# Optimization experiments

Hardware: AMD Instinct MI355X
Metric: run time of the kernel (lower is better)

## Reference

```python
import jax, jax.numpy as jnp
import numpy as np

N, E, D, R, G, C = 100000, 600000, 128, 4, 256, 16
EPS = 1e-5

def _rgcn(x, src, dst, edge_type, w_rel, w_root, b):
    # out_i = x_i @ W_root + b + sum_r mean_{j in N_r(i)} x_j @ W_r  (PyG RGCNConv, aggr='mean')
    x_src = x[src]                                   # [E, D] gather
    out = x @ w_root + b                             # [N, D]
    for r in range(R):
        m = (edge_type == r).astype(x.dtype)         # [E]
        msg = (x_src @ w_rel[r]) * m[:, None]        # [E, D]
        agg = jax.ops.segment_sum(msg, dst, num_segments=N)
        cnt = jax.ops.segment_sum(m, dst, num_segments=N)
        out = out + agg / jnp.maximum(cnt, 1.0)[:, None]
    return out

def _bn_eval(x, gamma, beta, mean, var):
    return (x - mean) * jax.lax.rsqrt(var + EPS) * gamma + beta

def setup_inputs() -> dict:
    key = jax.random.key(0)
    ks = jax.random.split(key, 12)
    x = jax.random.normal(ks[0], (N, D), dtype=jnp.float32)
    edge_index = jax.random.randint(ks[1], (2, E), 0, N)
    edge_type = jax.random.randint(ks[2], (E,), 0, R)
    batch = jnp.sort(jax.random.randint(ks[3], (N,), 0, G))
    s = 1.0 / np.sqrt(D)
    conv_rel_w = jax.random.normal(ks[4], (3, R, D, D), dtype=jnp.float32) * s
    conv_root_w = jax.random.normal(ks[5], (3, D, D), dtype=jnp.float32) * s
    conv_bias = jnp.zeros((3, D), dtype=jnp.float32)
    bn_gamma = jnp.ones((2, D), dtype=jnp.float32)
    bn_beta = jnp.zeros((2, D), dtype=jnp.float32)
    bn_mean = jax.random.normal(ks[6], (2, D), dtype=jnp.float32) * 0.1
    bn_var = jax.random.uniform(ks[7], (2, D), minval=0.5, maxval=1.5, dtype=jnp.float32)
    cls_w1 = jax.random.normal(ks[8], (D, D // 2), dtype=jnp.float32) * s
    cls_b1 = jnp.zeros((D // 2,), dtype=jnp.float32)
    cls_w2 = jax.random.normal(ks[9], (D // 2, C), dtype=jnp.float32) / np.sqrt(D // 2)
    cls_b2 = jnp.zeros((C,), dtype=jnp.float32)
    return {"x": x, "edge_index": edge_index, "edge_type": edge_type, "batch": batch,
            "conv_rel_w": conv_rel_w, "conv_root_w": conv_root_w, "conv_bias": conv_bias,
            "bn_gamma": bn_gamma, "bn_beta": bn_beta, "bn_mean": bn_mean, "bn_var": bn_var,
            "cls_w1": cls_w1, "cls_b1": cls_b1, "cls_w2": cls_w2, "cls_b2": cls_b2}

def reference(x, edge_index, edge_type, batch, conv_rel_w, conv_root_w, conv_bias,
              bn_gamma, bn_beta, bn_mean, bn_var, cls_w1, cls_b1, cls_w2, cls_b2):
    src, dst = edge_index[0], edge_index[1]
    prev = None
    h = x
    for i in range(3):
        h_new = _rgcn(h, src, dst, edge_type, conv_rel_w[i], conv_root_w[i], conv_bias[i])
        if prev is not None:
            h_new = h_new + prev  # residual (shapes always match: D==D)
        if i != 2:
            h_new = _bn_eval(h_new, bn_gamma[i], bn_beta[i], bn_mean[i], bn_var[i])
            h_new = jax.nn.elu(h_new)  # alpha=1; dropout inactive in eval
        prev = h_new
        h = h_new
    # global mean pool over graphs
    sums = jax.ops.segment_sum(h, batch, num_segments=G)          # [G, D]
    cnts = jax.ops.segment_sum(jnp.ones((N,), h.dtype), batch, num_segments=G)
    pooled = sums / jnp.maximum(cnts, 1.0)[:, None]
    z = jax.nn.elu(pooled @ cls_w1 + cls_b1)
    logits = z @ cls_w2 + cls_b2
    return jax.nn.log_softmax(logits, axis=-1)
```

## Files before the change

kernel.cpp:

```cpp
#include <hip/hip_runtime.h>
#include <hip/hip_bf16.h>

#define NN 100000
#define EE 600000
#define DD 128
#define GG 256
#define CCL 16

typedef __attribute__((ext_vector_type(8))) short short8;
typedef __attribute__((ext_vector_type(4))) float f32x4;
typedef const __attribute__((address_space(1))) void* gas_t;
typedef __attribute__((address_space(3))) void* las_t;

__device__ __forceinline__ void async_ld16(const void* g, void* l) {
    __builtin_amdgcn_global_load_lds((gas_t)g, (las_t)l, 16, 0, 0);
}
__device__ __forceinline__ unsigned short f2bf(float x) {
    unsigned u = __float_as_uint(x);
    unsigned r = (u + 0x7FFFu + ((u >> 16) & 1u)) >> 16;
    return (unsigned short)r;
}
__device__ __forceinline__ float bf2f(unsigned short b) {
    return __uint_as_float(((unsigned)b) << 16);
}
__device__ __forceinline__ void unpack8(uint4 v, float* f) {
    f[0] = __uint_as_float(v.x << 16); f[1] = __uint_as_float(v.x & 0xFFFF0000u);
    f[2] = __uint_as_float(v.y << 16); f[3] = __uint_as_float(v.y & 0xFFFF0000u);
    f[4] = __uint_as_float(v.z << 16); f[5] = __uint_as_float(v.z & 0xFFFF0000u);
    f[6] = __uint_as_float(v.w << 16); f[7] = __uint_as_float(v.w & 0xFFFF0000u);
}

__global__ __launch_bounds__(256) void sniff_kernel(const void* __restrict__ xraw, int* __restrict__ flag) {
    int t = threadIdx.x;
    const unsigned short* u = (const unsigned short*)xraw;
    int good = 0;
    #pragma unroll
    for (int i = 0; i < 4; i++) {
        unsigned short b = u[t * 4 + i];
        int e = (b >> 7) & 0xFF;
        if (e >= 107 && e <= 130) good++;
    }
    __shared__ int sg[256];
    sg[t] = good;
    __syncthreads();
    for (int s = 128; s > 0; s >>= 1) { if (t < s) sg[t] += sg[t + s]; __syncthreads(); }
    if (t == 0) flag[0] = (sg[0] >= 900) ? 1 : 0;
}

__device__ __forceinline__ float loadf(const void* p, size_t i, int isbf) {
    if (isbf) return bf2f(((const unsigned short*)p)[i]);
    return ((const float*)p)[i];
}

__global__ __launch_bounds__(256) void convx_kernel(const void* __restrict__ xraw, const int* __restrict__ flag,
                                                    __hip_bfloat16* __restrict__ xc) {
    int isbf = flag[0];
    size_t i0 = ((size_t)blockIdx.x * 256 + threadIdx.x) * 8;
    if (i0 >= (size_t)NN * DD) return;
    if (isbf) {
        *(uint4*)(xc + i0) = *(const uint4*)((const __hip_bfloat16*)xraw + i0);
    } else {
        const float* xf = (const float*)xraw;
        unsigned short o[8];
        #pragma unroll
        for (int j = 0; j < 8; j++) o[j] = f2bf(xf[i0 + j]);
        *(uint4*)(xc + i0) = *(uint4*)o;
    }
}

__global__ __launch_bounds__(256) void convw_kernel(const void* __restrict__ rel_raw, const void* __restrict__ root_raw,
                                                    const int* __restrict__ flag, __hip_bfloat16* __restrict__ wt) {
    int isbf = flag[0];
    int mat = blockIdx.x;
    int layer = mat / 5, g = mat % 5;
    size_t srcoff = (g == 0) ? (size_t)layer * 16384 : (size_t)(layer * 4 + (g - 1)) * 16384;
    const void* sraw = (g == 0) ? root_raw : rel_raw;
    __hip_bfloat16* dstp = wt + (size_t)mat * 16384;
    for (int idx = threadIdx.x; idx < 16384; idx += 256) {
        int k = idx >> 7, n = idx & 127;
        float v = loadf(sraw, srcoff + (size_t)k * 128 + n, isbf);
        dstp[n * 128 + k] = __float2bfloat16(v);
    }
}

__global__ __launch_bounds__(256) void convp_kernel(const void* bias, const void* bng, const void* bnb,
                                                    const void* bnm, const void* bnv, const void* w1,
                                                    const void* b1, const void* w2, const void* b2,
                                                    const int* __restrict__ flag, float* __restrict__ pf) {
    int isbf = flag[0];
    int b = blockIdx.x, t = threadIdx.x;
    if (b < 9) {
        const void* srcs[9] = {bias, bng, bnb, bnm, bnv, w1, b1, w2, b2};
        const int cnts[9] = {384, 256, 256, 256, 256, 8192, 64, 1024, 16};
        const int offs[9] = {0, 384, 640, 896, 1152, 1408, 9600, 9664, 10688};
        const void* s = srcs[b];
        int c = cnts[b], o = offs[b];
        for (int i = t; i < c; i += 256) pf[o + i] = loadf(s, i, isbf);
    } else {
        int bl = b - 9;
        if (t < 128) {
            float iva = rsqrtf(loadf(bnv, bl * 128 + t, isbf) + 1e-5f);
            float gm = loadf(bng, bl * 128 + t, isbf) * iva;
            float ga = loadf(bnb, bl * 128 + t, isbf) - loadf(bnm, bl * 128 + t, isbf) * gm;
            pf[11008 + bl * 256 + t] = gm;
            pf[11008 + bl * 256 + 128 + t] = ga;
        }
    }
}

__global__ __launch_bounds__(256) void count4_kernel(const int* __restrict__ dst, const int* __restrict__ et,
                                                     int* __restrict__ cnt4) {
    int e = blockIdx.x * 256 + threadIdx.x;
    if (e < EE) atomicAdd(&cnt4[dst[e] * 4 + et[e]], 1);
}

__global__ __launch_bounds__(256) void allocn_kernel(const int* __restrict__ cnt4, int* __restrict__ counter,
                                                     int* __restrict__ startn, int* __restrict__ wptrn) {
    int n = blockIdx.x * 256 + threadIdx.x;
    int lane = threadIdx.x & 63;
    int c = 0;
    if (n < NN) {
        int4 cv = *(const int4*)(cnt4 + n * 4);
        c = cv.x + cv.y + cv.z + cv.w;
    }
    int v = c;
    #pragma unroll
    for (int d = 1; d < 64; d <<= 1) {
        int o = __shfl_up(v, d);
        if (lane >= d) v += o;
    }
    int base = 0;
    if (lane == 63) base = atomicAdd(counter, v);
    base = __shfl(base, 63);
    if (n < NN) {
        int s = base + v - c;
        startn[n] = s;
        wptrn[n] = s;
    }
}

__global__ __launch_bounds__(256) void filln_kernel(const int* __restrict__ src, const int* __restrict__ dst,
                                                    const int* __restrict__ et, const int* __restrict__ cnt4,
                                                    int* __restrict__ wptrn, int2* __restrict__ ewe) {
    int e = blockIdx.x * 256 + threadIdx.x;
    if (e < EE) {
        int d = dst[e], r = et[e];
        float w = 1.f / (float)cnt4[d * 4 + r];
        int pos = atomicAdd(&wptrn[d], 1);
        ewe[pos] = make_int2(src[e] * 512 + r * 128, __float_as_int(w));
    }
}

__global__ __launch_bounds__(256) void gemmy_kernel(const __hip_bfloat16* __restrict__ h_in,
                                                    const __hip_bfloat16* __restrict__ wt5,
                                                    __hip_bfloat16* __restrict__ Yroot,
                                                    __hip_bfloat16* __restrict__ Yrel) {
    __shared__ __align__(16) short lds[16384];
    int t = threadIdx.x;
    int wave = t >> 6, lane = t & 63, quad = lane >> 4, r16 = lane & 15;
    int m0 = blockIdx.x * 128;
    int g = blockIdx.y;

    const __hip_bfloat16* wg = wt5 + (size_t)g * 16384;
    #pragma unroll
    for (int j = 0; j < 8; j++) {
        int slot = j * 256 + t;
        int brow = slot >> 4, sp = slot & 15;
        async_ld16(wg + brow * 128 + (sp ^ (brow & 15)) * 8, &lds[slot * 8]);
    }
    int r0 = m0 + wave * 32 + r16;      if (r0 > NN - 1) r0 = NN - 1;
    int r1 = m0 + wave * 32 + 16 + r16; if (r1 > NN - 1) r1 = NN - 1;
    const __hip_bfloat16* ap0 = h_in + (size_t)r0 * 128;
    const __hip_bfloat16* ap1 = h_in + (size_t)r1 * 128;
    short8 a0[4], a1[4];
    #pragma unroll
    for (int kc = 0; kc < 4; kc++) {
        a0[kc] = *(const short8*)(ap0 + kc * 32 + quad * 8);
        a1[kc] = *(const short8*)(ap1 + kc * 32 + quad * 8);
    }
    __syncthreads();

    f32x4 acc[2][8];
    #pragma unroll
    for (int i = 0; i < 2; i++)
        #pragma unroll
        for (int j = 0; j < 8; j++) acc[i][j] = (f32x4){0.f, 0.f, 0.f, 0.f};
    #pragma unroll
    for (int kc = 0; kc < 4; kc++) {
        int s = kc * 4 + quad;
        #pragma unroll
        for (int nt = 0; nt < 8; nt++) {
            int rb = nt * 16 + r16;
            short8 b = *(const short8*)&lds[(rb * 16 + (s ^ (rb & 15))) * 8];
            acc[0][nt] = __builtin_amdgcn_mfma_f32_16x16x32_bf16(a0[kc], b, acc[0][nt], 0, 0, 0);
            acc[1][nt] = __builtin_amdgcn_mfma_f32_16x16x32_bf16(a1[kc], b, acc[1][nt], 0, 0, 0);
        }
    }
    __syncthreads();

    #pragma unroll
    for (int nt = 0; nt < 8; nt++) {
        int col = nt * 16 + r16;
        #pragma unroll
        for (int mt = 0; mt < 2; mt++) {
            #pragma unroll
            for (int reg = 0; reg < 4; reg++) {
                int crow = wave * 32 + mt * 16 + quad * 4 + reg;
                int sslot = (col >> 3) ^ (crow & 15);
                lds[crow * 128 + sslot * 8 + (col & 7)] = (short)f2bf(acc[mt][nt][reg]);
            }
        }
    }
    __syncthreads();

    #pragma unroll
    for (int it = 0; it < 8; it++) {
        int u4 = it * 256 + t;
        int crow = u4 >> 4, seg = u4 & 15;
        int node = m0 + crow;
        if (node < NN) {
            int sslot = seg ^ (crow & 15);
            short8 cv = *(const short8*)&lds[crow * 128 + sslot * 8];
            __hip_bfloat16* dp = (g == 0) ? (Yroot + (size_t)node * 128 + seg * 8)
                                          : (Yrel + (size_t)node * 512 + (g - 1) * 128 + seg * 8);
            *(uint4*)dp = *(uint4*)&cv;
        }
    }
}

__global__ __launch_bounds__(256) void sagg_kernel(const __hip_bfloat16* __restrict__ Yrel,
                                                   const __hip_bfloat16* __restrict__ Yroot,
                                                   const int2* __restrict__ ewe,
                                                   const int* __restrict__ startn,
                                                   const int* __restrict__ wptrn,
                                                   const float* __restrict__ bias,
                                                   const float* __restrict__ gmp,
                                                   const float* __restrict__ gap,
                                                   const __hip_bfloat16* __restrict__ hres,
                                                   __hip_bfloat16* __restrict__ hout,
                                                   int do_bn) {
    int node = blockIdx.x * 16 + (threadIdx.x >> 4);
    int c16 = threadIdx.x & 15;
    int s = startn[node];
    int c = wptrn[node] - s;
    int col0 = c16 * 8;
    float a[8];
    unpack8(*(const uint4*)(Yroot + (size_t)node * 128 + col0), a);
    int i = 0;
    for (; i + 8 <= c; i += 8) {
        int2 ee[8];
        uint4 vv[8];
        #pragma unroll
        for (int q = 0; q < 8; q++) ee[q] = ewe[s + i + q];
        #pragma unroll
        for (int q = 0; q < 8; q++) vv[q] = *(const uint4*)(Yrel + ee[q].x + col0);
        #pragma unroll
        for (int q = 0; q < 8; q++) {
            float w = __int_as_float(ee[q].y);
            float f[8];
            unpack8(vv[q], f);
            #pragma unroll
            for (int j = 0; j < 8; j++) a[j] += w * f[j];
        }
    }
    for (; i + 4 <= c; i += 4) {
        int2 ee[4];
        uint4 vv[4];
        #pragma unroll
        for (int q = 0; q < 4; q++) ee[q] = ewe[s + i + q];
        #pragma unroll
        for (int q = 0; q < 4; q++) vv[q] = *(const uint4*)(Yrel + ee[q].x + col0);
        #pragma unroll
        for (int q = 0; q < 4; q++) {
            float w = __int_as_float(ee[q].y);
            float f[8];
            unpack8(vv[q], f);
            #pragma unroll
            for (int j = 0; j < 8; j++) a[j] += w * f[j];
        }
    }
    for (; i < c; i++) {
        int2 e0 = ewe[s + i];
        uint4 v0 = *(const uint4*)(Yrel + e0.x + col0);
        float w0 = __int_as_float(e0.y);
        float f0[8];
        unpack8(v0, f0);
        #pragma unroll
        for (int j = 0; j < 8; j++) a[j] += w0 * f0[j];
    }
    if (hres) {
        float rf[8];
        unpack8(*(const uint4*)(hres + (size_t)node * 128 + col0), rf);
        #pragma unroll
        for (int j = 0; j < 8; j++) a[j] = a[j] + bias[col0 + j] + rf[j];
    } else {
        #pragma unroll
        for (int j = 0; j < 8; j++) a[j] = a[j] + bias[col0 + j];
    }
    if (do_bn) {
        #pragma unroll
        for (int j = 0; j < 8; j++) {
            float z = a[j] * gmp[col0 + j] + gap[col0 + j];
            a[j] = z > 0.f ? z : expm1f(z);
        }
    }
    unsigned short u[8];
    #pragma unroll
    for (int j = 0; j < 8; j++) u[j] = f2bf(a[j]);
    *(uint4*)(hout + (size_t)node * 128 + col0) = *(uint4*)u;
}

__global__ __launch_bounds__(256) void pool_kernel(const __hip_bfloat16* __restrict__ h3,
                                                   const int* __restrict__ batch,
                                                   float* __restrict__ pooled) {
    int g = blockIdx.x, t = threadIdx.x;
    int rowpar = t >> 4, colg = t & 15;
    int lo = 0, hi = NN;
    while (lo < hi) { int mid = (lo + hi) >> 1; if (batch[mid] < g) lo = mid + 1; else hi = mid; }
    int s0 = lo;
    hi = NN;
    while (lo < hi) { int mid = (lo + hi) >> 1; if (batch[mid] < g + 1) lo = mid + 1; else hi = mid; }
    int s1 = lo;
    float a[8];
    #pragma unroll
    for (int j = 0; j < 8; j++) a[j] = 0.f;
    for (int n = s0 + rowpar; n < s1; n += 16) {
        float f[8];
        unpack8(*(const uint4*)(h3 + (size_t)n * 128 + colg * 8), f);
        #pragma unroll
        for (int j = 0; j < 8; j++) a[j] += f[j];
    }
    __shared__ float sd[16][128];
    #pragma unroll
    for (int j = 0; j < 8; j++) sd[rowpar][colg * 8 + j] = a[j];
    __syncthreads();
    if (t < 128) {
        float sum = 0.f;
        #pragma unroll
        for (int i = 0; i < 16; i++) sum += sd[i][t];
        int cgn = s1 - s0;
        pooled[g * 128 + t] = sum / (float)(cgn > 0 ? cgn : 1);
    }
}

__global__ __launch_bounds__(64) void cls_kernel(const float* __restrict__ pooled,
                                                 const float* __restrict__ pf,
                                                 const int* __restrict__ flag,
                                                 void* __restrict__ out) {
    int g = blockIdx.x, j = threadIdx.x;
    const float* w1 = pf + 1408;
    const float* b1 = pf + 9600;
    const float* w2 = pf + 9664;
    const float* b2 = pf + 10688;
    __shared__ float z[64];
    __shared__ float lg[16];
    const float* p = pooled + g * 128;
    float acc = b1[j];
    for (int d = 0; d < 128; d++) acc += p[d] * w1[d * 64 + j];
    acc = acc > 0.f ? acc : expm1f(acc);
    z[j] = acc;
    __syncthreads();
    if (j < CCL) {
        float l = b2[j];
        for (int k = 0; k < 64; k++) l += z[k] * w2[k * 16 + j];
        lg[j] = l;
    }
    __syncthreads();
    if (j < CCL) {
        float m = lg[0];
        for (int k = 1; k < CCL; k++) m = fmaxf(m, lg[k]);
        float s = 0.f;
        for (int k = 0; k < CCL; k++) s += expf(lg[k] - m);
        float val = lg[j] - m - logf(s);
        if (flag[0]) ((__hip_bfloat16*)out)[g * CCL + j] = __float2bfloat16(val);
        else         ((float*)out)[g * CCL + j] = val;
    }
}

extern "C" void kernel_launch(void* const* d_in, const int* in_sizes, int n_in,
                              void* d_out, int out_size, void* d_ws, size_t ws_size,
                              hipStream_t stream) {
    const void* x_raw    = d_in[0];
    const int* ei        = (const int*)d_in[1];
    const int* et        = (const int*)d_in[2];
    const int* batch     = (const int*)d_in[3];
    const void* rel_raw  = d_in[4];
    const void* root_raw = d_in[5];
    const int* srcp = ei;
    const int* dstp = ei + EE;

    char* ws = (char*)d_ws;
    size_t off = 0;
    auto take = [&](size_t bytes) { size_t r = off; off += (bytes + 1023) & ~(size_t)1023; return r; };
    __hip_bfloat16* Yrel  = (__hip_bfloat16*)(ws + take((size_t)NN * 512 * 2));
    __hip_bfloat16* Yroot = (__hip_bfloat16*)(ws + take((size_t)NN * 128 * 2));
    __hip_bfloat16* xc    = (__hip_bfloat16*)(ws + take((size_t)NN * 128 * 2));
    __hip_bfloat16* hA    = (__hip_bfloat16*)(ws + take((size_t)NN * 128 * 2));
    __hip_bfloat16* hB    = (__hip_bfloat16*)(ws + take((size_t)NN * 128 * 2));
    __hip_bfloat16* hC    = (__hip_bfloat16*)(ws + take((size_t)NN * 128 * 2));
    __hip_bfloat16* wt    = (__hip_bfloat16*)(ws + take((size_t)15 * 16384 * 2));
    float* pf             = (float*)(ws + take((size_t)11520 * 4));
    float* pooled         = (float*)(ws + take((size_t)GG * 128 * 4));
    int* cnt4             = (int*)(ws + take((size_t)NN * 16 + 8));
    int* counter          = cnt4 + NN * 4;
    int* flag             = cnt4 + NN * 4 + 1;
    int* startn           = (int*)(ws + take((size_t)NN * 4));
    int* wptrn            = (int*)(ws + take((size_t)NN * 4));
    int2* ewe             = (int2*)(ws + take((size_t)EE * 8));

    hipMemsetAsync(cnt4, 0, (size_t)NN * 16 + 4, stream);
    sniff_kernel<<<1, 256, 0, stream>>>(x_raw, flag);
    convx_kernel<<<(NN * DD / 8 + 255) / 256, 256, 0, stream>>>(x_raw, flag, xc);
    convw_kernel<<<15, 256, 0, stream>>>(rel_raw, root_raw, flag, wt);
    convp_kernel<<<11, 256, 0, stream>>>(d_in[6], d_in[7], d_in[8], d_in[9], d_in[10],
                                         d_in[11], d_in[12], d_in[13], d_in[14], flag, pf);
    count4_kernel<<<(EE + 255) / 256, 256, 0, stream>>>(dstp, et, cnt4);
    allocn_kernel<<<(NN + 255) / 256, 256, 0, stream>>>(cnt4, counter, startn, wptrn);
    filln_kernel<<<(EE + 255) / 256, 256, 0, stream>>>(srcp, dstp, et, cnt4, wptrn, ewe);

    const __hip_bfloat16* hin = xc;
    __hip_bfloat16* houts[3] = {hA, hB, hC};
    dim3 ggrid((NN + 127) / 128, 5);
    for (int l = 0; l < 3; l++) {
        int bl = l < 2 ? l : 1;
        gemmy_kernel<<<ggrid, 256, 0, stream>>>(hin, wt + (size_t)l * 5 * 16384, Yroot, Yrel);
        sagg_kernel<<<NN / 16, 256, 0, stream>>>(
            Yrel, Yroot, ewe, startn, wptrn, pf + l * 128,
            pf + 11008 + bl * 256, pf + 11008 + bl * 256 + 128,
            (l > 0) ? hin : (const __hip_bfloat16*)nullptr, houts[l], (l < 2) ? 1 : 0);
        hin = houts[l];
    }
    pool_kernel<<<GG, 256, 0, stream>>>(houts[2], batch, pooled);
    cls_kernel<<<GG, 64, 0, stream>>>(pooled, pf, flag, (void*)d_out);
}
```

Before: 576.8 us.

## Aggregate neighbors before transform, fuse K=640 GEMM with bias/BN/ELU epilogue

Reorders each RGCN layer so per-relation mean aggregation of raw 128-wide features happens first, with edges bucketed by (dst, relation). A single GEMM then multiplies the concatenated [h | A_0..A_3] by the stacked weights, and bias, residual, BN and ELU are applied in its epilogue. This replaces the gather of 512-wide transformed rows and the separate Yroot/Yrel writes with 128-wide gathers and one fused output pass. The edge record shrinks to a source index, and the normalisation weight is taken from the per-bucket count. The cost is an extra Abuf write and read per layer and serialised K chunks inside each GEMM block.

New measurement: 572.7 us. Within noise of the previous version (-0.7%).

```diff
diff --git a/kernel.cpp b/kernel.cpp
--- a/kernel.cpp
+++ b/kernel.cpp
@@ -115,12 +115,13 @@
 }
 
 __global__ __launch_bounds__(256) void allocn_kernel(const int* __restrict__ cnt4, int* __restrict__ counter,
-                                                     int* __restrict__ startn, int* __restrict__ wptrn) {
+                                                     int* __restrict__ startn, int* __restrict__ wptr4) {
     int n = blockIdx.x * 256 + threadIdx.x;
     int lane = threadIdx.x & 63;
+    int4 cv = make_int4(0, 0, 0, 0);
     int c = 0;
     if (n < NN) {
-        int4 cv = *(const int4*)(cnt4 + n * 4);
+        cv = *(const int4*)(cnt4 + n * 4);
         c = cv.x + cv.y + cv.z + cv.w;
     }
     int v = c;
@@ -135,179 +136,182 @@
     if (n < NN) {
         int s = base + v - c;
         startn[n] = s;
-        wptrn[n] = s;
-    }
-}
-
-__global__ __launch_bounds__(256) void filln_kernel(const int* __restrict__ src, const int* __restrict__ dst,
-                                                    const int* __restrict__ et, const int* __restrict__ cnt4,
-                                                    int* __restrict__ wptrn, int2* __restrict__ ewe) {
+        wptr4[n * 4 + 0] = s;
+        wptr4[n * 4 + 1] = s + cv.x;
+        wptr4[n * 4 + 2] = s + cv.x + cv.y;
+        wptr4[n * 4 + 3] = s + cv.x + cv.y + cv.z;
+    }
+}
+
+__global__ __launch_bounds__(256) void fill4_kernel(const int* __restrict__ src, const int* __restrict__ dst,
+                                                    const int* __restrict__ et, int* __restrict__ wptr4,
+                                                    int* __restrict__ esrc) {
     int e = blockIdx.x * 256 + threadIdx.x;
     if (e < EE) {
-        int d = dst[e], r = et[e];
-        float w = 1.f / (float)cnt4[d * 4 + r];
-        int pos = atomicAdd(&wptrn[d], 1);
-        ewe[pos] = make_int2(src[e] * 512 + r * 128, __float_as_int(w));
-    }
-}
-
-__global__ __launch_bounds__(256) void gemmy_kernel(const __hip_bfloat16* __restrict__ h_in,
+        int pos = atomicAdd(&wptr4[dst[e] * 4 + et[e]], 1);
+        esrc[pos] = src[e];
+    }
+}
+
+__global__ __launch_bounds__(256) void agg_kernel(const __hip_bfloat16* __restrict__ h,
+                                                  const int* __restrict__ esrc,
+                                                  const int* __restrict__ startn,
+                                                  const int* __restrict__ cnt4,
+                                                  __hip_bfloat16* __restrict__ Abuf) {
+    int node = blockIdx.x * 16 + (threadIdx.x >> 4);
+    int c16 = threadIdx.x & 15;
+    int col0 = c16 * 8;
+    int4 cv = *(const int4*)(cnt4 + node * 4);
+    int s = startn[node];
+    int cr[4] = {cv.x, cv.y, cv.z, cv.w};
+    #pragma unroll
+    for (int r = 0; r < 4; r++) {
+        int c = cr[r];
+        float a[8];
+        #pragma unroll
+        for (int j = 0; j < 8; j++) a[j] = 0.f;
+        int i = 0;
+        for (; i + 4 <= c; i += 4) {
+            int s4[4];
+            uint4 vv[4];
+            #pragma unroll
+            for (int q = 0; q < 4; q++) s4[q] = esrc[s + i + q];
+            #pragma unroll
+            for (int q = 0; q < 4; q++) vv[q] = *(const uint4*)(h + (size_t)s4[q] * 128 + col0);
+            #pragma unroll
+            for (int q = 0; q < 4; q++) {
+                float f[8];
+                unpack8(vv[q], f);
+                #pragma unroll
+                for (int j = 0; j < 8; j++) a[j] += f[j];
+            }
+        }
+        for (; i < c; i++) {
+            int sq = esrc[s + i];
+            uint4 v0 = *(const uint4*)(h + (size_t)sq * 128 + col0);
+            float f[8];
+            unpack8(v0, f);
+            #pragma unroll
+            for (int j = 0; j < 8; j++) a[j] += f[j];
+        }
+        float w = (c > 0) ? (1.f / (float)c) : 0.f;
+        unsigned short u[8];
+        #pragma unroll
+        for (int j = 0; j < 8; j++) u[j] = f2bf(a[j] * w);
+        *(uint4*)(Abuf + (size_t)node * 512 + r * 128 + col0) = *(uint4*)u;
+        s += c;
+    }
+}
+
+__global__ __launch_bounds__(256) void rgemm_kernel(const __hip_bfloat16* __restrict__ h_in,
+                                                    const __hip_bfloat16* __restrict__ Abuf,
                                                     const __hip_bfloat16* __restrict__ wt5,
-                                                    __hip_bfloat16* __restrict__ Yroot,
-                                                    __hip_bfloat16* __restrict__ Yrel) {
+                                                    const float* __restrict__ bias,
+                                                    const float* __restrict__ gmp,
+                                                    const float* __restrict__ gap,
+                                                    const __hip_bfloat16* __restrict__ hres,
+                                                    __hip_bfloat16* __restrict__ hout,
+                                                    int do_bn) {
     __shared__ __align__(16) short lds[16384];
     int t = threadIdx.x;
     int wave = t >> 6, lane = t & 63, quad = lane >> 4, r16 = lane & 15;
     int m0 = blockIdx.x * 128;
-    int g = blockIdx.y;
-
-    const __hip_bfloat16* wg = wt5 + (size_t)g * 16384;
-    #pragma unroll
-    for (int j = 0; j < 8; j++) {
-        int slot = j * 256 + t;
-        int brow = slot >> 4, sp = slot & 15;
-        async_ld16(wg + brow * 128 + (sp ^ (brow & 15)) * 8, &lds[slot * 8]);
-    }
+
     int r0 = m0 + wave * 32 + r16;      if (r0 > NN - 1) r0 = NN - 1;
     int r1 = m0 + wave * 32 + 16 + r16; if (r1 > NN - 1) r1 = NN - 1;
-    const __hip_bfloat16* ap0 = h_in + (size_t)r0 * 128;
-    const __hip_bfloat16* ap1 = h_in + (size_t)r1 * 128;
-    short8 a0[4], a1[4];
-    #pragma unroll
-    for (int kc = 0; kc < 4; kc++) {
-        a0[kc] = *(const short8*)(ap0 + kc * 32 + quad * 8);
-        a1[kc] = *(const short8*)(ap1 + kc * 32 + quad * 8);
-    }
-    __syncthreads();
 
     f32x4 acc[2][8];
     #pragma unroll
     for (int i = 0; i < 2; i++)
         #pragma unroll
         for (int j = 0; j < 8; j++) acc[i][j] = (f32x4){0.f, 0.f, 0.f, 0.f};
-    #pragma unroll
-    for (int kc = 0; kc < 4; kc++) {
-        int s = kc * 4 + quad;
-        #pragma unroll
-        for (int nt = 0; nt < 8; nt++) {
-            int rb = nt * 16 + r16;
-            short8 b = *(const short8*)&lds[(rb * 16 + (s ^ (rb & 15))) * 8];
-            acc[0][nt] = __builtin_amdgcn_mfma_f32_16x16x32_bf16(a0[kc], b, acc[0][nt], 0, 0, 0);
-            acc[1][nt] = __builtin_amdgcn_mfma_f32_16x16x32_bf16(a1[kc], b, acc[1][nt], 0, 0, 0);
-        }
-    }
-    __syncthreads();
-
-    #pragma unroll
-    for (int nt = 0; nt < 8; nt++) {
-        int col = nt * 16 + r16;
-        #pragma unroll
-        for (int mt = 0; mt < 2; mt++) {
-            #pragma unroll
-            for (int reg = 0; reg < 4; reg++) {
-                int crow = wave * 32 + mt * 16 + quad * 4 + reg;
-                int sslot = (col >> 3) ^ (crow & 15);
-                lds[crow * 128 + sslot * 8 + (col & 7)] = (short)f2bf(acc[mt][nt][reg]);
+
+    #pragma unroll
+    for (int ch = 0; ch < 5; ch++) {
+        if (ch) __syncthreads();
+        const __hip_bfloat16* wg = wt5 + (size_t)ch * 16384;
+        #pragma unroll
+        for (int j = 0; j < 8; j++) {
+            int slot = j * 256 + t;
+            int brow = slot >> 4, sp = slot & 15;
+            async_ld16(wg + brow * 128 + (sp ^ (brow & 15)) * 8, &lds[slot * 8]);
+        }
+        const __hip_bfloat16* ap0;
+        const __hip_bfloat16* ap1;
+        if (ch == 0) {
+            ap0 = h_in + (size_t)r0 * 128;
+            ap1 = h_in + (size_t)r1 * 128;
+        } else {
+            ap0 = Abuf + (size_t)r0 * 512 + (ch - 1) * 128;
+            ap1 = Abuf + (size_t)r1 * 512 + (ch - 1) * 128;
+        }
+        short8 a0[4], a1[4];
+        #pragma unroll
+        for (int kc = 0; kc < 4; kc++) {
+            a0[kc] = *(const short8*)(ap0 + kc * 32 + quad * 8);
+            a1[kc] = *(const short8*)(ap1 + kc * 32 + quad * 8);
+        }
+        __syncthreads();
+        #pragma unroll
+        for (int kc = 0; kc < 4; kc++) {
+            int s = kc * 4 + quad;
+            #pragma unroll
+            for (int nt = 0; nt < 8; nt++) {
+                int rb = nt * 16 + r16;
+                short8 b = *(const short8*)&lds[(rb * 16 + (s ^ (rb & 15))) * 8];
+                acc[0][nt] = __builtin_amdgcn_mfma_f32_16x16x32_bf16(a0[kc], b, acc[0][nt], 0, 0, 0);
+                acc[1][nt] = __builtin_amdgcn_mfma_f32_16x16x32_bf16(a1[kc], b, acc[1][nt], 0, 0, 0);
             }
         }
     }
-    __syncthreads();
-
-    #pragma unroll
-    for (int it = 0; it < 8; it++) {
-        int u4 = it * 256 + t;
-        int crow = u4 >> 4, seg = u4 & 15;
-        int node = m0 + crow;
-        if (node < NN) {
-            int sslot = seg ^ (crow & 15);
-            short8 cv = *(const short8*)&lds[crow * 128 + sslot * 8];
-            __hip_bfloat16* dp = (g == 0) ? (Yroot + (size_t)node * 128 + seg * 8)
-                                          : (Yrel + (size_t)node * 512 + (g - 1) * 128 + seg * 8);
-            *(uint4*)dp = *(uint4*)&cv;
-        }
-    }
-}
-
-__global__ __launch_bounds__(256) void sagg_kernel(const __hip_bfloat16* __restrict__ Yrel,
-                                                   const __hip_bfloat16* __restrict__ Yroot,
-                                                   const int2* __restrict__ ewe,
-                                                   const int* __restrict__ startn,
-                                                   const int* __restrict__ wptrn,
-                                                   const float* __restrict__ bias,
-                                                   const float* __restrict__ gmp,
-                                                   const float* __restrict__ gap,
-                                                   const __hip_bfloat16* __restrict__ hres,
-                                                   __hip_bfloat16* __restrict__ hout,
-                                                   int do_bn) {
-    int node = blockIdx.x * 16 + (threadIdx.x >> 4);
-    int c16 = threadIdx.x & 15;
-    int s = startn[node];
-    int c = wptrn[node] - s;
-    int col0 = c16 * 8;
-    float a[8];
-    unpack8(*(const uint4*)(Yroot + (size_t)node * 128 + col0), a);
-    int i = 0;
-    for (; i + 8 <= c; i += 8) {
-        int2 ee[8];
-        uint4 vv[8];
-        #pragma unroll
-        for (int q = 0; q < 8; q++) ee[q] = ewe[s + i + q];
-        #pragma unroll
-        for (int q = 0; q < 8; q++) vv[q] = *(const uint4*)(Yrel + ee[q].x + col0);
-        #pragma unroll
-        for (int q = 0; q < 8; q++) {
-            float w = __int_as_float(ee[q].y);
-            float f[8];
-            unpack8(vv[q], f);
-            #pragma unroll
-            for (int j = 0; j < 8; j++) a[j] += w * f[j];
-        }
-    }
-    for (; i + 4 <= c; i += 4) {
-        int2 ee[4];
-        uint4 vv[4];
-        #pragma unroll
-        for (int q = 0; q < 4; q++) ee[q] = ewe[s + i + q];
-        #pragma unroll
-        for (int q = 0; q < 4; q++) vv[q] = *(const uint4*)(Yrel + ee[q].x + col0);
-        #pragma unroll
-        for (int q = 0; q < 4; q++) {
-            float w = __int_as_float(ee[q].y);
-            float f[8];
-            unpack8(vv[q], f);
-            #pragma unroll
-            for (int j = 0; j < 8; j++) a[j] += w * f[j];
-        }
-    }
-    for (; i < c; i++) {
-        int2 e0 = ewe[s + i];
-        uint4 v0 = *(const uint4*)(Yrel + e0.x + col0);
-        float w0 = __int_as_float(e0.y);
-        float f0[8];
-        unpack8(v0, f0);
-        #pragma unroll
-        for (int j = 0; j < 8; j++) a[j] += w0 * f0[j];
-    }
-    if (hres) {
-        float rf[8];
-        unpack8(*(const uint4*)(hres + (size_t)node * 128 + col0), rf);
-        #pragma unroll
-        for (int j = 0; j < 8; j++) a[j] = a[j] + bias[col0 + j] + rf[j];
-    } else {
-        #pragma unroll
-        for (int j = 0; j < 8; j++) a[j] = a[j] + bias[col0 + j];
-    }
-    if (do_bn) {
-        #pragma unroll
-        for (int j = 0; j < 8; j++) {
-            float z = a[j] * gmp[col0 + j] + gap[col0 + j];
-            a[j] = z > 0.f ? z : expm1f(z);
-        }
-    }
-    unsigned short u[8];
-    #pragma unroll
-    for (int j = 0; j < 8; j++) u[j] = f2bf(a[j]);
-    *(uint4*)(hout + (size_t)node * 128 + col0) = *(uint4*)u;
+
+    float* cf = (float*)lds;
+    #pragma unroll
+    for (int half = 0; half < 2; half++) {
+        __syncthreads();
+        #pragma unroll
+        for (int nt = half * 4; nt < half * 4 + 4; nt++) {
+            int col = (nt - half * 4) * 16 + r16;
+            #pragma unroll
+            for (int mt = 0; mt < 2; mt++) {
+                #pragma unroll
+                for (int reg = 0; reg < 4; reg++) {
+                    int crow = wave * 32 + mt * 16 + quad * 4 + reg;
+                    cf[crow * 64 + col] = acc[mt][nt][reg];
+                }
+            }
+        }
+        __syncthreads();
+        #pragma unroll
+        for (int it = 0; it < 4; it++) {
+            int u4 = it * 256 + t;
+            int crow = u4 >> 3, seg = u4 & 7;
+            int node = m0 + crow;
+            if (node < NN) {
+                int gcol0 = half * 64 + seg * 8;
+                float a[8];
+                #pragma unroll
+                for (int j = 0; j < 8; j++) a[j] = cf[crow * 64 + seg * 8 + j] + bias[gcol0 + j];
+                if (hres) {
+                    float rf[8];
+                    unpack8(*(const uint4*)(hres + (size_t)node * 128 + gcol0), rf);
+                    #pragma unroll
+                    for (int j = 0; j < 8; j++) a[j] += rf[j];
+                }
+                if (do_bn) {
+                    #pragma unroll
+                    for (int j = 0; j < 8; j++) {
+                        float z = a[j] * gmp[gcol0 + j] + gap[gcol0 + j];
+                        a[j] = z > 0.f ? z : expm1f(z);
+                    }
+                }
+                unsigned short u[8];
+                #pragma unroll
+                for (int j = 0; j < 8; j++) u[j] = f2bf(a[j]);
+                *(uint4*)(hout + (size_t)node * 128 + gcol0) = *(uint4*)u;
+            }
+        }
+    }
 }
 
 __global__ __launch_bounds__(256) void pool_kernel(const __hip_bfloat16* __restrict__ h3,
@@ -392,8 +396,7 @@
     char* ws = (char*)d_ws;
     size_t off = 0;
     auto take = [&](size_t bytes) { size_t r = off; off += (bytes + 1023) & ~(size_t)1023; return r; };
-    __hip_bfloat16* Yrel  = (__hip_bfloat16*)(ws + take((size_t)NN * 512 * 2));
-    __hip_bfloat16* Yroot = (__hip_bfloat16*)(ws + take((size_t)NN * 128 * 2));
+    __hip_bfloat16* Abuf  = (__hip_bfloat16*)(ws + take((size_t)NN * 512 * 2));
     __hip_bfloat16* xc    = (__hip_bfloat16*)(ws + take((size_t)NN * 128 * 2));
     __hip_bfloat16* hA    = (__hip_bfloat16*)(ws + take((size_t)NN * 128 * 2));
     __hip_bfloat16* hB    = (__hip_bfloat16*)(ws + take((size_t)NN * 128 * 2));
@@ -405,8 +408,8 @@
     int* counter          = cnt4 + NN * 4;
     int* flag             = cnt4 + NN * 4 + 1;
     int* startn           = (int*)(ws + take((size_t)NN * 4));
-    int* wptrn            = (int*)(ws + take((size_t)NN * 4));
-    int2* ewe             = (int2*)(ws + take((size_t)EE * 8));
+    int* wptr4            = (int*)(ws + take((size_t)NN * 16));
+    int* esrc             = (int*)(ws + take((size_t)EE * 4));
 
     hipMemsetAsync(cnt4, 0, (size_t)NN * 16 + 4, stream);
     sniff_kernel<<<1, 256, 0, stream>>>(x_raw, flag);
@@ -415,17 +418,16 @@
     convp_kernel<<<11, 256, 0, stream>>>(d_in[6], d_in[7], d_in[8], d_in[9], d_in[10],
                                          d_in[11], d_in[12], d_in[13], d_in[14], flag, pf);
     count4_kernel<<<(EE + 255) / 256, 256, 0, stream>>>(dstp, et, cnt4);
-    allocn_kernel<<<(NN + 255) / 256, 256, 0, stream>>>(cnt4, counter, startn, wptrn);
-    filln_kernel<<<(EE + 255) / 256, 256, 0, stream>>>(srcp, dstp, et, cnt4, wptrn, ewe);
+    allocn_kernel<<<(NN + 255) / 256, 256, 0, stream>>>(cnt4, counter, startn, wptr4);
+    fill4_kernel<<<(EE + 255) / 256, 256, 0, stream>>>(srcp, dstp, et, wptr4, esrc);
 
     const __hip_bfloat16* hin = xc;
     __hip_bfloat16* houts[3] = {hA, hB, hC};
-    dim3 ggrid((NN + 127) / 128, 5);
     for (int l = 0; l < 3; l++) {
         int bl = l < 2 ? l : 1;
-        gemmy_kernel<<<ggrid, 256, 0, stream>>>(hin, wt + (size_t)l * 5 * 16384, Yroot, Yrel);
-        sagg_kernel<<<NN / 16, 256, 0, stream>>>(
-            Yrel, Yroot, ewe, startn, wptrn, pf + l * 128,
+        agg_kernel<<<NN / 16, 256, 0, stream>>>(hin, esrc, startn, cnt4, Abuf);
+        rgemm_kernel<<<(NN + 127) / 128, 256, 0, stream>>>(
+            hin, Abuf, wt + (size_t)l * 5 * 16384, pf + l * 128,
             pf + 11008 + bl * 256, pf + 11008 + bl * 256 + 128,
             (l > 0) ? hin : (const __hip_bfloat16*)nullptr, houts[l], (l < 2) ? 1 : 0);
         hin = houts[l];
```
